# Kernel optimization log

Measured on AMD Instinct MI355X. Metric: run time of the kernel, lower is better.

Reference implementation:

```python
import jax, jax.numpy as jnp
import numpy as np


def _pairwise_l2(set1, set2):
    # set1: [B, N, C], set2: [B, M, C] -> [B, N, M] Euclidean distances.
    # Equivalent to ||a - b||_2 computed via the expanded quadratic form,
    # avoiding the O(B*N*M*C) broadcasted-difference intermediate.
    sq1 = jnp.sum(set1 * set1, axis=-1)  # [B, N]
    sq2 = jnp.sum(set2 * set2, axis=-1)  # [B, M]
    inner = jnp.einsum('bnc,bmc->bnm', set1, set2)  # [B, N, M]
    d2 = sq1[:, :, None] + sq2[:, None, :] - 2.0 * inner
    return jnp.sqrt(jnp.maximum(d2, 0.0))


def reference(set1, set2):
    # mode == Hausdorff.average
    if set1.ndim == 2:
        set1 = set1[None]
    if set2.ndim == 2:
        set2 = set2[None]
    distances = _pairwise_l2(set1, set2)  # [B, N, M]
    term_1 = jnp.mean(jnp.min(distances, axis=2), axis=1)  # [B]
    term_2 = jnp.mean(jnp.min(distances, axis=1), axis=1)  # [B]
    res = term_1 + term_2
    if res.shape[0] == 1:
        res = jnp.squeeze(res, axis=0)
    return res


def setup_inputs() -> dict:
    key = jax.random.key(0)
    k1, k2 = jax.random.split(key)
    B, N, M, C = 8, 4096, 4096, 128
    set1 = jax.random.normal(k1, (B, N, C), dtype=jnp.float32)
    set2 = jax.random.normal(k2, (B, M, C), dtype=jnp.float32)
    return {"set1": set1, "set2": set2}
```

## Files before the change

### kernel.cpp

```cpp
#include <hip/hip_runtime.h>

#define B_ 8
#define N_ 4096
#define M_ 4096
#define C_ 128
#define BN_ (B_ * N_)
#define BM_ (B_ * M_)

typedef __attribute__((ext_vector_type(8))) short bf16x8;
typedef __attribute__((ext_vector_type(4))) float floatx4;
typedef __attribute__((ext_vector_type(8))) unsigned short ushort8;

__device__ __forceinline__ unsigned short f2bf(float x) {
    unsigned int u = __float_as_uint(x);
    u += 0x7FFFu + ((u >> 16) & 1u);
    return (unsigned short)(u >> 16);
}

__device__ __forceinline__ void gl2lds16(const void* g, void* l) {
    __builtin_amdgcn_global_load_lds(
        (const __attribute__((address_space(1))) void*)g,
        (__attribute__((address_space(3))) void*)l, 16, 0, 0);
}

__global__ __launch_bounds__(256) void prep_kernel(
    const float* __restrict__ S1, const float* __restrict__ S2,
    unsigned int* __restrict__ minbuf, float* __restrict__ norms,
    unsigned short* __restrict__ bfA, unsigned short* __restrict__ bfB,
    float* __restrict__ out) {
    const int lane = threadIdx.x & 63;
    const int w    = threadIdx.x >> 6;
    const int gw   = blockIdx.x * 4 + w;
    const int r4   = lane >> 4;
    const int g4   = lane & 15;
    const int row  = gw * 4 + r4;

    const float* src = (row < BN_) ? S1 + (size_t)row * C_
                                   : S2 + (size_t)(row - BN_) * C_;
    float4 v0 = ((const float4*)src)[g4 * 2];
    float4 v1 = ((const float4*)src)[g4 * 2 + 1];

    float s = v0.x*v0.x + v0.y*v0.y + v0.z*v0.z + v0.w*v0.w
            + v1.x*v1.x + v1.y*v1.y + v1.z*v1.z + v1.w*v1.w;
    s += __shfl_xor(s, 1, 64);
    s += __shfl_xor(s, 2, 64);
    s += __shfl_xor(s, 4, 64);
    s += __shfl_xor(s, 8, 64);

    ushort8 o;
    o[0] = f2bf(v0.x); o[1] = f2bf(v0.y); o[2] = f2bf(v0.z); o[3] = f2bf(v0.w);
    o[4] = f2bf(v1.x); o[5] = f2bf(v1.y); o[6] = f2bf(v1.z); o[7] = f2bf(v1.w);

    unsigned short* dst = (row < BN_) ? bfA + (size_t)row * C_
                                      : bfB + (size_t)(row - BN_) * C_;
    *(ushort8*)&dst[(g4 ^ (row & 15)) * 8] = o;

    if (g4 == 0) { norms[row] = s; minbuf[row] = 0x7F800000u; }
    if (blockIdx.x == 0 && threadIdx.x < B_) out[threadIdx.x] = 0.f;
}

__global__ __launch_bounds__(256, 2) void hausdorff_mfma(
    const unsigned short* __restrict__ Abf, const unsigned short* __restrict__ Bbf,
    const float* __restrict__ asq_g, const float* __restrict__ bsq_g,
    unsigned int* __restrict__ rowmin, unsigned int* __restrict__ colmin) {

    __shared__ unsigned short A_lds[128 * 128];
    __shared__ unsigned short B_lds[2][64 * 128];

    const int b     = blockIdx.z;
    const int row0  = blockIdx.x * 128;
    const int panel = blockIdx.y;
    const int tid   = threadIdx.x;
    const int lane  = tid & 63;
    const int w     = tid >> 6;
    const int lm    = lane & 15;
    const int quad  = lane >> 4;
    const int wrow  = (w >> 1) * 64;
    const int qc    = (w & 1) * 32;

    const unsigned short* Aws = Abf + ((size_t)b * N_ + row0) * C_;
    const unsigned short* Bws = Bbf + ((size_t)b * M_ + panel * 1024) * C_;

    #pragma unroll
    for (int k = 0; k < 8; ++k) {
        const int off = w * 4096 + k * 512;
        gl2lds16(Aws + off + lane * 8, &A_lds[off]);
    }
    #pragma unroll
    for (int k = 0; k < 4; ++k) {
        const int off = w * 2048 + k * 512;
        gl2lds16(Bws + off + lane * 8, &B_lds[0][off]);
    }

    float sa[16];
    #pragma unroll
    for (int i = 0; i < 4; ++i) {
        float4 t = *(const float4*)&asq_g[(size_t)b * N_ + row0 + wrow + 16 * i + 4 * quad];
        sa[4*i+0] = t.x; sa[4*i+1] = t.y; sa[4*i+2] = t.z; sa[4*i+3] = t.w;
    }

    float rv[16];
    #pragma unroll
    for (int v = 0; v < 16; ++v) rv[v] = 1e30f;

    __syncthreads();

    bf16x8 af[4][4];
    #pragma unroll
    for (int i = 0; i < 4; ++i)
        #pragma unroll
        for (int c = 0; c < 4; ++c)
            af[i][c] = *(const bf16x8*)
                &A_lds[(wrow + 16 * i + lm) * 128 + (((c * 4 + quad) ^ lm) * 8)];

    for (int it = 0; it < 16; ++it) {
        const int cur = it & 1;
        if (it < 15) {
            const unsigned short* Bt = Bws + (size_t)(it + 1) * 64 * C_;
            #pragma unroll
            for (int k = 0; k < 4; ++k) {
                const int off = w * 2048 + k * 512;
                gl2lds16(Bt + off + lane * 8, &B_lds[cur ^ 1][off]);
            }
        }
        const int colbase = panel * 1024 + it * 64;
        const float sb0 = bsq_g[(size_t)b * M_ + colbase + qc + lm];
        const float sb1 = bsq_g[(size_t)b * M_ + colbase + qc + 16 + lm];

        bf16x8 bf[2][4];
        #pragma unroll
        for (int j = 0; j < 2; ++j)
            #pragma unroll
            for (int c = 0; c < 4; ++c)
                bf[j][c] = *(const bf16x8*)
                    &B_lds[cur][(qc + 16 * j + lm) * 128 + (((c * 4 + quad) ^ lm) * 8)];

        floatx4 acc[4][2] = {};
        #pragma unroll
        for (int c = 0; c < 4; ++c)
            #pragma unroll
            for (int i = 0; i < 4; ++i)
                #pragma unroll
                for (int j = 0; j < 2; ++j)
                    acc[i][j] = __builtin_amdgcn_mfma_f32_16x16x32_bf16(
                        af[i][c], bf[j][c], acc[i][j], 0, 0, 0);

        float cv0 = 1e30f, cv1 = 1e30f;
        #pragma unroll
        for (int i = 0; i < 4; ++i)
            #pragma unroll
            for (int reg = 0; reg < 4; ++reg) {
                const int v = 4 * i + reg;
                float d0 = fmaf(-2.0f, acc[i][0][reg], sa[v] + sb0);
                float d1 = fmaf(-2.0f, acc[i][1][reg], sa[v] + sb1);
                rv[v] = fminf(rv[v], fminf(d0, d1));
                cv0 = fminf(cv0, d0);
                cv1 = fminf(cv1, d1);
            }
        cv0 = fminf(cv0, __shfl_xor(cv0, 16, 64));
        cv0 = fminf(cv0, __shfl_xor(cv0, 32, 64));
        cv1 = fminf(cv1, __shfl_xor(cv1, 16, 64));
        cv1 = fminf(cv1, __shfl_xor(cv1, 32, 64));
        if (quad == 0) {
            atomicMin(&colmin[(size_t)b * M_ + colbase + qc + lm],
                      __float_as_uint(fmaxf(cv0, 0.f)));
            atomicMin(&colmin[(size_t)b * M_ + colbase + qc + 16 + lm],
                      __float_as_uint(fmaxf(cv1, 0.f)));
        }
        __syncthreads();
    }

    #pragma unroll
    for (int s = 1; s < 16; s <<= 1)
        #pragma unroll
        for (int v = 0; v < 16; ++v)
            rv[v] = fminf(rv[v], __shfl_xor(rv[v], s, 64));
    if (lm == 0) {
        #pragma unroll
        for (int v = 0; v < 16; ++v)
            atomicMin(&rowmin[(size_t)b * N_ + row0 + wrow + 16 * (v >> 2) +
                              4 * quad + (v & 3)],
                      __float_as_uint(fmaxf(rv[v], 0.f)));
    }
}

__global__ __launch_bounds__(256) void hausdorff_reduce(
    const unsigned int* __restrict__ rowmin,
    const unsigned int* __restrict__ colmin, float* __restrict__ out) {
    __shared__ float ws4[4];
    const int b    = blockIdx.x >> 3;
    const int part = blockIdx.x & 7;
    const int base = part * 512;
    float s = 0.f;
    for (int i = base + threadIdx.x; i < base + 512; i += 256)
        s += sqrtf(fmaxf(__uint_as_float(rowmin[(size_t)b * N_ + i]), 0.f)) * (1.f / N_)
           + sqrtf(fmaxf(__uint_as_float(colmin[(size_t)b * M_ + i]), 0.f)) * (1.f / M_);
    #pragma unroll
    for (int off = 32; off > 0; off >>= 1) s += __shfl_down(s, off, 64);
    if ((threadIdx.x & 63) == 0) ws4[threadIdx.x >> 6] = s;
    __syncthreads();
    if (threadIdx.x == 0)
        atomicAdd(&out[b], ws4[0] + ws4[1] + ws4[2] + ws4[3]);
}

extern "C" void kernel_launch(void* const* d_in, const int* in_sizes, int n_in,
                              void* d_out, int out_size, void* d_ws, size_t ws_size,
                              hipStream_t stream) {
    const float* s1 = (const float*)d_in[0];
    const float* s2 = (const float*)d_in[1];
    float* out = (float*)d_out;

    unsigned int* rowmin = (unsigned int*)d_ws;
    unsigned int* colmin = rowmin + BN_;
    float* norms         = (float*)(colmin + BM_);
    unsigned short* bfA  = (unsigned short*)(norms + BN_ + BM_);
    unsigned short* bfB  = bfA + (size_t)BN_ * C_;

    prep_kernel<<<(BN_ + BM_) / 16, 256, 0, stream>>>(
        s1, s2, rowmin, norms, bfA, bfB, out);

    dim3 grid(N_ / 128, M_ / 1024, B_);
    hausdorff_mfma<<<grid, 256, 0, stream>>>(
        bfA, bfB, norms, norms + BN_, rowmin, colmin);

    hausdorff_reduce<<<B_ * 8, 256, 0, stream>>>(rowmin, colmin, out);
}
```

Baseline: 132.9 us.

## Pre-swizzle bf16 operands into MFMA fragment layout and load directly to registers

The prep kernel now writes bf16 data in per-lane MFMA fragment order, so the main kernel loads A and B fragments straight from global memory into registers. This removes LDS staging and all __syncthreads. B fragments are double-buffered in registers across unrolled iterations. Each block now covers 2048 columns instead of 1024, halving the grid along M, and the reduce kernel uses one block per batch with a plain store instead of atomics. The cost is heavier direct global/L2 traffic with no LDS reuse across waves, and fewer blocks in flight.

```diff
diff --git a/kernel.cpp b/kernel.cpp
--- a/kernel.cpp
+++ b/kernel.cpp
@@ -17,55 +17,55 @@
     return (unsigned short)(u >> 16);
 }
 
-__device__ __forceinline__ void gl2lds16(const void* g, void* l) {
-    __builtin_amdgcn_global_load_lds(
-        (const __attribute__((address_space(1))) void*)g,
-        (__attribute__((address_space(3))) void*)l, 16, 0, 0);
-}
 
 __global__ __launch_bounds__(256) void prep_kernel(
     const float* __restrict__ S1, const float* __restrict__ S2,
     unsigned int* __restrict__ minbuf, float* __restrict__ norms,
-    unsigned short* __restrict__ bfA, unsigned short* __restrict__ bfB,
-    float* __restrict__ out) {
+    unsigned short* __restrict__ Afrag, unsigned short* __restrict__ Bfrag) {
     const int lane = threadIdx.x & 63;
     const int w    = threadIdx.x >> 6;
-    const int gw   = blockIdx.x * 4 + w;
-    const int r4   = lane >> 4;
-    const int g4   = lane & 15;
-    const int row  = gw * 4 + r4;
-
-    const float* src = (row < BN_) ? S1 + (size_t)row * C_
-                                   : S2 + (size_t)(row - BN_) * C_;
-    float4 v0 = ((const float4*)src)[g4 * 2];
-    float4 v1 = ((const float4*)src)[g4 * 2 + 1];
-
-    float s = v0.x*v0.x + v0.y*v0.y + v0.z*v0.z + v0.w*v0.w
-            + v1.x*v1.x + v1.y*v1.y + v1.z*v1.z + v1.w*v1.w;
-    s += __shfl_xor(s, 1, 64);
-    s += __shfl_xor(s, 2, 64);
-    s += __shfl_xor(s, 4, 64);
-    s += __shfl_xor(s, 8, 64);
-
-    ushort8 o;
-    o[0] = f2bf(v0.x); o[1] = f2bf(v0.y); o[2] = f2bf(v0.z); o[3] = f2bf(v0.w);
-    o[4] = f2bf(v1.x); o[5] = f2bf(v1.y); o[6] = f2bf(v1.z); o[7] = f2bf(v1.w);
-
-    unsigned short* dst = (row < BN_) ? bfA + (size_t)row * C_
-                                      : bfB + (size_t)(row - BN_) * C_;
-    *(ushort8*)&dst[(g4 ^ (row & 15)) * 8] = o;
-
-    if (g4 == 0) { norms[row] = s; minbuf[row] = 0x7F800000u; }
-    if (blockIdx.x == 0 && threadIdx.x < B_) out[threadIdx.x] = 0.f;
+    const int lm   = lane & 15;
+    const int quad = lane >> 4;
+
+    const int unit  = blockIdx.x * 4 + w;
+    const int batch = unit >> 9;
+    const int rem   = unit & 511;
+    const int isB   = rem >> 8;
+    const int q     = rem & 255;
+    const int t     = q >> 2;
+    const int h     = (q >> 1) & 1;
+    const int j     = q & 1;
+    const int m     = t * 64 + h * 32 + j * 16 + lm;
+
+    const float* src = (isB ? S2 : S1) + ((size_t)batch * 4096 + m) * C_;
+    unsigned short* dst = (isB ? Bfrag : Afrag) + (size_t)batch * (4096 * C_)
+                        + (size_t)(((t * 2 + h) * 2 + j) * 4) * 64 * 8;
+
+    float s = 0.f;
+    #pragma unroll
+    for (int c = 0; c < 4; ++c) {
+        float4 v0 = *(const float4*)(src + c * 32 + quad * 8);
+        float4 v1 = *(const float4*)(src + c * 32 + quad * 8 + 4);
+        s += v0.x*v0.x + v0.y*v0.y + v0.z*v0.z + v0.w*v0.w
+           + v1.x*v1.x + v1.y*v1.y + v1.z*v1.z + v1.w*v1.w;
+        ushort8 o;
+        o[0] = f2bf(v0.x); o[1] = f2bf(v0.y); o[2] = f2bf(v0.z); o[3] = f2bf(v0.w);
+        o[4] = f2bf(v1.x); o[5] = f2bf(v1.y); o[6] = f2bf(v1.z); o[7] = f2bf(v1.w);
+        *(ushort8*)&dst[(size_t)(c * 64 + lane) * 8] = o;
+    }
+    s += __shfl_xor(s, 16, 64);
+    s += __shfl_xor(s, 32, 64);
+    if (quad == 0) {
+        const int gr = (isB ? BN_ : 0) + batch * 4096 + m;
+        norms[gr]  = s;
+        minbuf[gr] = 0x7F800000u;
+    }
 }
 
 __global__ __launch_bounds__(256, 2) void hausdorff_mfma(
-    const unsigned short* __restrict__ Abf, const unsigned short* __restrict__ Bbf,
+    const unsigned short* __restrict__ Afrag, const unsigned short* __restrict__ Bfrag,
     const float* __restrict__ asq_g, const float* __restrict__ bsq_g,
     unsigned int* __restrict__ rowmin, unsigned int* __restrict__ colmin) {
-
-    __shared__ unsigned short A_lds[128 * 128];
-    __shared__ unsigned short B_lds[2][64 * 128];
 
     const int b     = blockIdx.z;
     const int row0  = blockIdx.x * 128;
@@ -76,21 +76,20 @@
     const int lm    = lane & 15;
     const int quad  = lane >> 4;
     const int wrow  = (w >> 1) * 64;
-    const int qc    = (w & 1) * 32;
-
-    const unsigned short* Aws = Abf + ((size_t)b * N_ + row0) * C_;
-    const unsigned short* Bws = Bbf + ((size_t)b * M_ + panel * 1024) * C_;
-
-    #pragma unroll
-    for (int k = 0; k < 8; ++k) {
-        const int off = w * 4096 + k * 512;
-        gl2lds16(Aws + off + lane * 8, &A_lds[off]);
-    }
-    #pragma unroll
-    for (int k = 0; k < 4; ++k) {
-        const int off = w * 2048 + k * 512;
-        gl2lds16(Bws + off + lane * 8, &B_lds[0][off]);
-    }
+    const int wch   = w & 1;
+
+    const unsigned short* Af = Afrag + (size_t)b * (4096 * C_);
+    const unsigned short* Bf = Bfrag + (size_t)b * (4096 * C_);
+    const int tA  = (row0 >> 6) + (w >> 1);
+    const int tB0 = panel * 32;
+
+    bf16x8 af[4][4];
+    #pragma unroll
+    for (int i = 0; i < 4; ++i)
+        #pragma unroll
+        for (int c = 0; c < 4; ++c)
+            af[i][c] = *(const bf16x8*)
+                &Af[(size_t)(((((tA * 2 + (i >> 1)) * 2 + (i & 1)) * 4 + c) * 64 + lane)) * 8];
 
     float sa[16];
     #pragma unroll
@@ -103,37 +102,20 @@
     #pragma unroll
     for (int v = 0; v < 16; ++v) rv[v] = 1e30f;
 
-    __syncthreads();
-
-    bf16x8 af[4][4];
-    #pragma unroll
-    for (int i = 0; i < 4; ++i)
-        #pragma unroll
-        for (int c = 0; c < 4; ++c)
-            af[i][c] = *(const bf16x8*)
-                &A_lds[(wrow + 16 * i + lm) * 128 + (((c * 4 + quad) ^ lm) * 8)];
-
-    for (int it = 0; it < 16; ++it) {
-        const int cur = it & 1;
-        if (it < 15) {
-            const unsigned short* Bt = Bws + (size_t)(it + 1) * 64 * C_;
-            #pragma unroll
-            for (int k = 0; k < 4; ++k) {
-                const int off = w * 2048 + k * 512;
-                gl2lds16(Bt + off + lane * 8, &B_lds[cur ^ 1][off]);
-            }
-        }
-        const int colbase = panel * 1024 + it * 64;
-        const float sb0 = bsq_g[(size_t)b * M_ + colbase + qc + lm];
-        const float sb1 = bsq_g[(size_t)b * M_ + colbase + qc + 16 + lm];
-
-        bf16x8 bf[2][4];
+    auto loadB = [&](bf16x8 (&d)[2][4], int it) {
+        const unsigned short* base =
+            &Bf[(size_t)(((tB0 + it) * 2 + wch) * 2) * 4 * 64 * 8];
         #pragma unroll
         for (int j = 0; j < 2; ++j)
             #pragma unroll
             for (int c = 0; c < 4; ++c)
-                bf[j][c] = *(const bf16x8*)
-                    &B_lds[cur][(qc + 16 * j + lm) * 128 + (((c * 4 + quad) ^ lm) * 8)];
+                d[j][c] = *(const bf16x8*)&base[(size_t)((j * 4 + c) * 64 + lane) * 8];
+    };
+
+    auto compute = [&](bf16x8 (&bfr)[2][4], int it) {
+        const int colbase = panel * 2048 + it * 64 + wch * 32;
+        const float sb0 = bsq_g[(size_t)b * M_ + colbase + lm];
+        const float sb1 = bsq_g[(size_t)b * M_ + colbase + 16 + lm];
 
         floatx4 acc[4][2] = {};
         #pragma unroll
@@ -143,7 +125,7 @@
                 #pragma unroll
                 for (int j = 0; j < 2; ++j)
                     acc[i][j] = __builtin_amdgcn_mfma_f32_16x16x32_bf16(
-                        af[i][c], bf[j][c], acc[i][j], 0, 0, 0);
+                        af[i][c], bfr[j][c], acc[i][j], 0, 0, 0);
 
         float cv0 = 1e30f, cv1 = 1e30f;
         #pragma unroll
@@ -162,12 +144,20 @@
         cv1 = fminf(cv1, __shfl_xor(cv1, 16, 64));
         cv1 = fminf(cv1, __shfl_xor(cv1, 32, 64));
         if (quad == 0) {
-            atomicMin(&colmin[(size_t)b * M_ + colbase + qc + lm],
+            atomicMin(&colmin[(size_t)b * M_ + colbase + lm],
                       __float_as_uint(fmaxf(cv0, 0.f)));
-            atomicMin(&colmin[(size_t)b * M_ + colbase + qc + 16 + lm],
+            atomicMin(&colmin[(size_t)b * M_ + colbase + 16 + lm],
                       __float_as_uint(fmaxf(cv1, 0.f)));
         }
-        __syncthreads();
+    };
+
+    bf16x8 bfP[2][4], bfQ[2][4];
+    loadB(bfP, 0);
+    for (int it2 = 0; it2 < 32; it2 += 2) {
+        loadB(bfQ, it2 + 1);
+        compute(bfP, it2);
+        if (it2 < 30) loadB(bfP, it2 + 2);
+        compute(bfQ, it2 + 1);
     }
 
     #pragma unroll
@@ -188,11 +178,9 @@
     const unsigned int* __restrict__ rowmin,
     const unsigned int* __restrict__ colmin, float* __restrict__ out) {
     __shared__ float ws4[4];
-    const int b    = blockIdx.x >> 3;
-    const int part = blockIdx.x & 7;
-    const int base = part * 512;
+    const int b = blockIdx.x;
     float s = 0.f;
-    for (int i = base + threadIdx.x; i < base + 512; i += 256)
+    for (int i = threadIdx.x; i < N_; i += 256)
         s += sqrtf(fmaxf(__uint_as_float(rowmin[(size_t)b * N_ + i]), 0.f)) * (1.f / N_)
            + sqrtf(fmaxf(__uint_as_float(colmin[(size_t)b * M_ + i]), 0.f)) * (1.f / M_);
     #pragma unroll
@@ -200,7 +188,7 @@
     if ((threadIdx.x & 63) == 0) ws4[threadIdx.x >> 6] = s;
     __syncthreads();
     if (threadIdx.x == 0)
-        atomicAdd(&out[b], ws4[0] + ws4[1] + ws4[2] + ws4[3]);
+        out[b] = ws4[0] + ws4[1] + ws4[2] + ws4[3];
 }
 
 extern "C" void kernel_launch(void* const* d_in, const int* in_sizes, int n_in,
@@ -210,18 +198,17 @@
     const float* s2 = (const float*)d_in[1];
     float* out = (float*)d_out;
 
-    unsigned int* rowmin = (unsigned int*)d_ws;
-    unsigned int* colmin = rowmin + BN_;
-    float* norms         = (float*)(colmin + BM_);
-    unsigned short* bfA  = (unsigned short*)(norms + BN_ + BM_);
-    unsigned short* bfB  = bfA + (size_t)BN_ * C_;
-
-    prep_kernel<<<(BN_ + BM_) / 16, 256, 0, stream>>>(
-        s1, s2, rowmin, norms, bfA, bfB, out);
-
-    dim3 grid(N_ / 128, M_ / 1024, B_);
+    unsigned int* rowmin  = (unsigned int*)d_ws;
+    unsigned int* colmin  = rowmin + BN_;
+    float* norms          = (float*)(colmin + BM_);
+    unsigned short* Afrag = (unsigned short*)(norms + BN_ + BM_);
+    unsigned short* Bfrag = Afrag + (size_t)BN_ * C_;
+
+    prep_kernel<<<1024, 256, 0, stream>>>(s1, s2, rowmin, norms, Afrag, Bfrag);
+
+    dim3 grid(N_ / 128, M_ / 2048, B_);
     hausdorff_mfma<<<grid, 256, 0, stream>>>(
-        bfA, bfB, norms, norms + BN_, rowmin, colmin);
-
-    hausdorff_reduce<<<B_ * 8, 256, 0, stream>>>(rowmin, colmin, out);
-}
+        Afrag, Bfrag, norms, norms + BN_, rowmin, colmin);
+
+    hausdorff_reduce<<<B_, 256, 0, stream>>>(rowmin, colmin, out);
+}
```

Result: faster. 130.1 us (-2.1%).
